# Performance work log

Hardware: AMD Instinct MI355X
Metric: run time of the kernel (lower is better)

## Reference

```python
import jax, jax.numpy as jnp
import numpy as np

N = 50000      # nodes
E = 600000     # edges
D = 128        # num_features == hidden_units
L = 4          # num_layers
C = 10         # num_classes
G = 512        # graphs in batch
BN_EPS = 1e-5


def setup_inputs() -> dict:
    key = jax.random.key(0)
    ks = jax.random.split(key, 10)
    x = jax.random.normal(ks[0], (N, D), dtype=jnp.float32)
    src = jax.random.randint(ks[1], (E,), 0, N)
    dst = jax.random.randint(ks[2], (E,), 0, N)
    edge_index = jnp.stack([src, dst]).astype(jnp.int64)
    batch = jnp.sort(jax.random.randint(ks[3], (N,), 0, G)).astype(jnp.int64)
    s = 1.0 / np.sqrt(D)
    Wc1 = jax.random.uniform(ks[4], (L, D, D), jnp.float32, -s, s)
    bc1 = jnp.zeros((L, D), jnp.float32)
    Wc2 = jax.random.uniform(ks[5], (L, D, D), jnp.float32, -s, s)
    bc2 = jnp.zeros((L, D), jnp.float32)
    g_mid = jnp.ones((L, D), jnp.float32)   # BN gamma inside conv MLP
    b_mid = jnp.zeros((L, D), jnp.float32)
    g_out = jnp.ones((L, D), jnp.float32)   # BN gamma after conv
    b_out = jnp.zeros((L, D), jnp.float32)
    fcW = jax.random.uniform(ks[6], (L + 1, D, C), jnp.float32, -s, s)
    fcb = jnp.zeros((L + 1, C), jnp.float32)
    return dict(x=x, edge_index=edge_index, batch=batch, Wc1=Wc1, bc1=bc1,
                Wc2=Wc2, bc2=bc2, g_mid=g_mid, b_mid=b_mid, g_out=g_out,
                b_out=b_out, fcW=fcW, fcb=fcb)


def _bn(h, gamma, beta):
    # training-mode BatchNorm1d over the node axis (biased variance)
    mu = h.mean(0)
    var = h.var(0)
    return (h - mu) * jax.lax.rsqrt(var + BN_EPS) * gamma + beta


def reference(x, edge_index, batch, Wc1, bc1, Wc2, bc2, g_mid, b_mid,
              g_out, b_out, fcW, fcb):
    src, dst = edge_index[0], edge_index[1]
    outs = [x]
    h = x
    for i in range(L):
        # GINConv (eps=0): nn( x + sum_{j in N(i)} x_j )
        agg = jax.ops.segment_sum(h[src], dst, num_segments=N)
        z = h + agg
        z = z @ Wc1[i] + bc1[i]
        z = jax.nn.relu(_bn(z, g_mid[i], b_mid[i]))
        z = z @ Wc2[i] + bc2[i]
        h = jax.nn.relu(_bn(z, g_out[i], b_out[i]))  # outer BN + ReLU
        outs.append(h)
    out = jnp.zeros((G, C), x.dtype)
    for i, o in enumerate(outs):
        pooled = jax.ops.segment_sum(o, batch, num_segments=G)  # [G, D]
        out = out + pooled @ fcW[i] + fcb[i]  # dropout p=0.0 -> identity
    return jax.nn.log_softmax(out, axis=-1)
```

## Files before the change

### kernel.cpp

```cpp
#include <hip/hip_runtime.h>
#include <hip/hip_bf16.h>

#define NN 50000
#define EE 600000
#define DD 128
#define LL 4
#define CC 10
#define GG 512
#define BN_EPS 1e-5f

typedef __attribute__((ext_vector_type(8))) short short8;
typedef __attribute__((ext_vector_type(4))) float f32x4;

__device__ __forceinline__ unsigned short f2b(float f) {
    union { float f; unsigned int u; } v; v.f = f;
    unsigned int u = v.u;
    unsigned int r = (u + 0x7fffu + ((u >> 16) & 1u)) >> 16;
    return (unsigned short)r;
}
__device__ __forceinline__ float b2f(unsigned short h) {
    union { unsigned int u; float f; } v; v.u = ((unsigned int)h) << 16;
    return v.f;
}


__global__ __launch_bounds__(256) void cvt_bf16(const float* __restrict__ in,
                                                unsigned short* __restrict__ out) {
    int i = blockIdx.x * 256 + threadIdx.x;
    float2 v = ((const float2*)in)[i];
    unsigned int o = (unsigned int)f2b(v.x) | ((unsigned int)f2b(v.y) << 16);
    ((unsigned int*)out)[i] = o;
}

__global__ __launch_bounds__(256) void prep_weights(const float* __restrict__ Wc1,
                                                    const float* __restrict__ Wc2,
                                                    unsigned short* __restrict__ WTb) {
    int idx = blockIdx.x * 256 + threadIdx.x;
    int mat = idx >> 14;
    int n = (idx >> 7) & 127;
    int k = idx & 127;
    const float* srcp = (mat < 4) ? (Wc1 + (size_t)mat * DD * DD)
                                  : (Wc2 + (size_t)(mat - 4) * DD * DD);
    WTb[idx] = f2b(srcp[k * DD + n]);
}


__global__ void hist_kernel(const int* __restrict__ idx, int* __restrict__ cnt, int n) {
    int i = blockIdx.x * blockDim.x + threadIdx.x;
    if (i < n) atomicAdd(&cnt[idx[i]], 1);
}

__global__ __launch_bounds__(256) void block_sums(const int* __restrict__ in,
                                                  int* __restrict__ bsums, int n) {
    __shared__ int red[256];
    int b = blockIdx.x, t = threadIdx.x;
    int base = b * 1024 + t * 4;
    int s = 0;
    if (base + 3 < n) {
        int4 v = *(const int4*)(in + base);
        s = v.x + v.y + v.z + v.w;
    } else {
        for (int i = 0; i < 4; ++i) if (base + i < n) s += in[base + i];
    }
    red[t] = s;
    __syncthreads();
    for (int off = 128; off > 0; off >>= 1) {
        if (t < off) red[t] += red[t + off];
        __syncthreads();
    }
    if (t == 0) bsums[b] = red[0];
}

__global__ __launch_bounds__(256) void scan_bsums(int* __restrict__ bsums, int nb) {
    __shared__ int red[256];
    int t = threadIdx.x;
    int v = (t < nb) ? bsums[t] : 0;
    red[t] = v;
    __syncthreads();
    for (int off = 1; off < 256; off <<= 1) {
        int u = (t >= off) ? red[t - off] : 0;
        __syncthreads();
        red[t] += u;
        __syncthreads();
    }
    if (t < nb) bsums[t] = red[t] - v;
    if (t == 0) bsums[nb] = red[255];
}

__global__ __launch_bounds__(256) void scan_final(const int* __restrict__ in,
                                                  const int* __restrict__ bsums,
                                                  int* __restrict__ out,
                                                  int* __restrict__ out2, int n) {
    __shared__ int red[256];
    int b = blockIdx.x, t = threadIdx.x;
    int base = b * 1024 + t * 4;
    int v[4];
    int s = 0;
#pragma unroll
    for (int i = 0; i < 4; ++i) {
        v[i] = (base + i < n) ? in[base + i] : 0;
        s += v[i];
    }
    red[t] = s;
    __syncthreads();
    for (int off = 1; off < 256; off <<= 1) {
        int u = (t >= off) ? red[t - off] : 0;
        __syncthreads();
        red[t] += u;
        __syncthreads();
    }
    int run = bsums[b] + red[t] - s;
#pragma unroll
    for (int i = 0; i < 4; ++i) {
        if (base + i < n) {
            out[base + i] = run;
            if (out2) out2[base + i] = run;
            run += v[i];
        }
    }
    if (b == (int)gridDim.x - 1 && t == 255) out[n] = run;
}

__global__ void fill_csr(const int* __restrict__ src, const int* __restrict__ dst,
                         int* __restrict__ cursor, int* __restrict__ csr) {
    int e = blockIdx.x * blockDim.x + threadIdx.x;
    if (e < EE) {
        int d = dst[e];
        int pos = atomicAdd(&cursor[d], 1);
        csr[pos] = src[e];
    }
}

__global__ void gptr_search(const int* __restrict__ batch, int* __restrict__ gptr) {
    int g = blockIdx.x * blockDim.x + threadIdx.x;
    if (g > GG) return;
    int lo = 0, hi = NN;
    while (lo < hi) {
        int mid = (lo + hi) >> 1;
        if (batch[mid] < g) lo = mid + 1; else hi = mid;
    }
    gptr[g] = lo;
}


template <bool BN>
__global__ __launch_bounds__(256) void aggregate_k(const unsigned short* __restrict__ hb,
                                                   const int* __restrict__ rowptr,
                                                   const int* __restrict__ csr,
                                                   const float* __restrict__ stats,
                                                   const float* __restrict__ gamma,
                                                   const float* __restrict__ beta,
                                                   unsigned short* __restrict__ outb) {
    int node = blockIdx.x * 4 + (threadIdx.x >> 6);
    if (node >= NN) return;
    int lane = threadIdx.x & 63;
    float A0 = 0.f, B0 = 0.f, A1 = 0.f, B1 = 0.f;
    if (BN) {
        int c0 = lane * 2, c1 = c0 + 1;
        float mu0 = stats[c0] * (1.0f / NN);
        float var0 = stats[DD + c0] * (1.0f / NN) - mu0 * mu0;
        A0 = gamma[c0] * rsqrtf(var0 + BN_EPS);
        B0 = beta[c0] - mu0 * A0;
        float mu1 = stats[c1] * (1.0f / NN);
        float var1 = stats[DD + c1] * (1.0f / NN) - mu1 * mu1;
        A1 = gamma[c1] * rsqrtf(var1 + BN_EPS);
        B1 = beta[c1] - mu1 * A1;
    }

    float ax, ay;
    {
        unsigned int u = ((const unsigned int*)(hb + (size_t)node * DD))[lane];
        float x = b2f((unsigned short)(u & 0xffff));
        float y = b2f((unsigned short)(u >> 16));
        if (BN) {
            x = fmaxf(0.f, fmaf(x, A0, B0));
            y = fmaxf(0.f, fmaf(y, A1, B1));
        }
        ax = x; ay = y;
    }

    int beg = rowptr[node], end = rowptr[node + 1];
    for (int e = beg; e < end; e += 8) {
        int m = end - e;
        int s[8];
#pragma unroll
        for (int i = 0; i < 8; ++i) s[i] = csr[e + ((i < m) ? i : 0)];
        unsigned int v[8];
#pragma unroll
        for (int i = 0; i < 8; ++i)
            v[i] = ((const unsigned int*)(hb + (size_t)s[i] * DD))[lane];
#pragma unroll
        for (int i = 0; i < 8; ++i) {
            if (i < m) {
                float x = b2f((unsigned short)(v[i] & 0xffff));
                float y = b2f((unsigned short)(v[i] >> 16));
                if (BN) {
                    x = fmaxf(0.f, fmaf(x, A0, B0));
                    y = fmaxf(0.f, fmaf(y, A1, B1));
                }
                ax += x; ay += y;
            }
        }
    }
    unsigned int o = (unsigned int)f2b(ax) | ((unsigned int)f2b(ay) << 16);
    ((unsigned int*)(outb + (size_t)node * DD))[lane] = o;
}


__global__ __launch_bounds__(256) void gemm_mfma(
    const unsigned short* __restrict__ Ab,
    const unsigned short* __restrict__ WTb,
    const float* __restrict__ bias,
    const float* __restrict__ bnStatsIn,
    const float* __restrict__ gamma, const float* __restrict__ beta,
    unsigned short* __restrict__ Outb,
    float* __restrict__ statsOut)
{
    __shared__ unsigned short As[128 * 128];
    __shared__ unsigned short Bs[128 * 128];
    __shared__ float AbnS[DD], BbnS[DD];
    __shared__ float colred[2][DD];

    const int tid = threadIdx.x;
    const int row0 = blockIdx.x * 128;
    const bool doBn = (bnStatsIn != nullptr);

    if (tid < DD) {
        colred[0][tid] = 0.f;
        colred[1][tid] = 0.f;
        if (doBn) {
            float mu = bnStatsIn[tid] * (1.0f / NN);
            float var = bnStatsIn[DD + tid] * (1.0f / NN) - mu * mu;
            float A = gamma[tid] * rsqrtf(var + BN_EPS);
            AbnS[tid] = A;
            BbnS[tid] = beta[tid] - mu * A;
        }
    }
    __syncthreads();

    const uint4* Bg = (const uint4*)WTb;
#pragma unroll
    for (int i = 0; i < 8; ++i) {
        int c = tid + i * 256;
        int row = c >> 4, seg = c & 15;
        uint4 v = Bg[c];
        int byte = (row * 256 + seg * 16) ^ ((row & 7) << 4);
        *(uint4*)((char*)Bs + byte) = v;
    }
#pragma unroll
    for (int i = 0; i < 8; ++i) {
        int c = tid + i * 256;
        int row = c >> 4, seg = c & 15;
        int gr = row0 + row;
        uint4 v = make_uint4(0u, 0u, 0u, 0u);
        if (gr < NN) v = ((const uint4*)(Ab + (size_t)gr * DD))[seg];
        if (doBn) {
            int k0 = seg * 8;
#pragma unroll
            for (int e = 0; e < 4; ++e) {
                unsigned int u = ((unsigned int*)&v)[e];
                int cidx = k0 + 2 * e;
                float lo = fmaxf(0.f, fmaf(b2f((unsigned short)(u & 0xffff)), AbnS[cidx], BbnS[cidx]));
                float hi = fmaxf(0.f, fmaf(b2f((unsigned short)(u >> 16)), AbnS[cidx + 1], BbnS[cidx + 1]));
                ((unsigned int*)&v)[e] = (unsigned int)f2b(lo) | ((unsigned int)f2b(hi) << 16);
            }
        }
        int byte = (row * 256 + seg * 16) ^ ((row & 7) << 4);
        *(uint4*)((char*)As + byte) = v;
    }
    __syncthreads();

    const int wave = tid >> 6, lane = tid & 63;
    const int fr = lane & 15, fq = lane >> 4;
    const int wr0 = wave * 32;

    f32x4 acc[2][8];
#pragma unroll
    for (int m = 0; m < 2; ++m)
#pragma unroll
        for (int n = 0; n < 8; ++n) acc[m][n] = (f32x4)0.f;

#pragma unroll
    for (int kk = 0; kk < 4; ++kk) {
        int kbyte = kk * 64 + fq * 16;
        short8 a[2], b[8];
#pragma unroll
        for (int m = 0; m < 2; ++m) {
            int row = wr0 + m * 16 + fr;
            a[m] = *(const short8*)((const char*)As + ((row * 256 + kbyte) ^ ((row & 7) << 4)));
        }
#pragma unroll
        for (int n = 0; n < 8; ++n) {
            int row = n * 16 + fr;
            b[n] = *(const short8*)((const char*)Bs + ((row * 256 + kbyte) ^ ((row & 7) << 4)));
        }
#pragma unroll
        for (int m = 0; m < 2; ++m)
#pragma unroll
            for (int n = 0; n < 8; ++n)
                acc[m][n] = __builtin_amdgcn_mfma_f32_16x16x32_bf16(a[m], b[n], acc[m][n], 0, 0, 0);
    }

    float bias_n[8], s[8], q[8];
#pragma unroll
    for (int n = 0; n < 8; ++n) {
        bias_n[n] = bias[n * 16 + fr];
        s[n] = 0.f;
        q[n] = 0.f;
    }
#pragma unroll
    for (int m = 0; m < 2; ++m) {
        int rbase = row0 + wr0 + m * 16 + fq * 4;
#pragma unroll
        for (int j = 0; j < 4; ++j) {
            int gr = rbase + j;
            if (gr < NN) {
#pragma unroll
                for (int n = 0; n < 8; ++n) {
                    float o = acc[m][n][j] + bias_n[n];
                    Outb[(size_t)gr * DD + n * 16 + fr] = f2b(o);
                    s[n] += o;
                    q[n] += o * o;
                }
            }
        }
    }
    if (statsOut) {
#pragma unroll
        for (int n = 0; n < 8; ++n) {
            s[n] += __shfl_xor(s[n], 16);
            s[n] += __shfl_xor(s[n], 32);
            q[n] += __shfl_xor(q[n], 16);
            q[n] += __shfl_xor(q[n], 32);
        }
        if (fq == 0) {
#pragma unroll
            for (int n = 0; n < 8; ++n) {
                atomicAdd(&colred[0][n * 16 + fr], s[n]);
                atomicAdd(&colred[1][n * 16 + fr], q[n]);
            }
        }
        __syncthreads();
        if (tid < DD) {
            atomicAdd(&statsOut[tid], colred[0][tid]);
            atomicAdd(&statsOut[DD + tid], colred[1][tid]);
        }
    }
}


__global__ __launch_bounds__(256) void bn_pool(const unsigned short* __restrict__ Z,
                                               const float* __restrict__ stats,
                                               const float* __restrict__ gamma,
                                               const float* __restrict__ beta,
                                               const int* __restrict__ gptr,
                                               float* __restrict__ pooledDst) {
    __shared__ float2 red[4][64];
    int g = blockIdx.x;
    int wave = threadIdx.x >> 6, lane = threadIdx.x & 63;
    int c0 = lane * 2, c1 = c0 + 1;
    float mu0 = stats[c0] * (1.0f / NN);
    float var0 = stats[DD + c0] * (1.0f / NN) - mu0 * mu0;
    float A0 = gamma[c0] * rsqrtf(var0 + BN_EPS);
    float B0 = beta[c0] - mu0 * A0;
    float mu1 = stats[c1] * (1.0f / NN);
    float var1 = stats[DD + c1] * (1.0f / NN) - mu1 * mu1;
    float A1 = gamma[c1] * rsqrtf(var1 + BN_EPS);
    float B1 = beta[c1] - mu1 * A1;

    float ax = 0.f, ay = 0.f;
    int beg = gptr[g], end = gptr[g + 1];
    for (int r = beg + wave; r < end; r += 4) {
        unsigned int u = ((const unsigned int*)(Z + (size_t)r * DD))[lane];
        ax += fmaxf(0.f, fmaf(b2f((unsigned short)(u & 0xffff)), A0, B0));
        ay += fmaxf(0.f, fmaf(b2f((unsigned short)(u >> 16)), A1, B1));
    }
    red[wave][lane] = make_float2(ax, ay);
    __syncthreads();
    if (threadIdx.x < 64) {
        float2 a = red[0][lane], b = red[1][lane], c = red[2][lane], d = red[3][lane];
        ((float2*)pooledDst)[(size_t)g * 64 + lane] =
            make_float2(a.x + b.x + c.x + d.x, a.y + b.y + c.y + d.y);
    }
}

__global__ __launch_bounds__(256) void pool_x(const float* __restrict__ src,
                                              const int* __restrict__ gptr,
                                              float* __restrict__ dst) {
    __shared__ float2 red[4][64];
    int g = blockIdx.x;
    int wave = threadIdx.x >> 6, lane = threadIdx.x & 63;
    float ax = 0.f, ay = 0.f;
    int beg = gptr[g], end = gptr[g + 1];
    for (int r = beg + wave; r < end; r += 4) {
        float2 v = ((const float2*)(src + (size_t)r * DD))[lane];
        ax += v.x; ay += v.y;
    }
    red[wave][lane] = make_float2(ax, ay);
    __syncthreads();
    if (threadIdx.x < 64) {
        float2 a = red[0][lane], b = red[1][lane], c = red[2][lane], d = red[3][lane];
        ((float2*)dst)[(size_t)g * 64 + lane] =
            make_float2(a.x + b.x + c.x + d.x, a.y + b.y + c.y + d.y);
    }
}


__global__ __launch_bounds__(64) void final_kernel(const float* __restrict__ pooled,
                                                   const float* __restrict__ fcW,
                                                   const float* __restrict__ fcb,
                                                   float* __restrict__ out) {
    int g = blockIdx.x;
    int lane = threadIdx.x;
    float acc[CC];
#pragma unroll
    for (int c = 0; c < CC; ++c) acc[c] = 0.f;
    for (int i = 0; i < LL + 1; ++i) {
        const float* P = pooled + ((size_t)i * GG + g) * DD;
        const float* Wf = fcW + (size_t)i * DD * CC;
        for (int k = lane; k < DD; k += 64) {
            float p = P[k];
            const float* wr = Wf + k * CC;
#pragma unroll
            for (int c = 0; c < CC; ++c) acc[c] = fmaf(p, wr[c], acc[c]);
        }
    }
#pragma unroll
    for (int c = 0; c < CC; ++c)
        for (int off = 32; off > 0; off >>= 1) acc[c] += __shfl_down(acc[c], off);
    if (lane == 0) {
#pragma unroll
        for (int c = 0; c < CC; ++c) {
            float b = 0.f;
            for (int i = 0; i < LL + 1; ++i) b += fcb[i * CC + c];
            acc[c] += b;
        }
        float m = acc[0];
#pragma unroll
        for (int c = 1; c < CC; ++c) m = fmaxf(m, acc[c]);
        float se = 0.f;
#pragma unroll
        for (int c = 0; c < CC; ++c) se += expf(acc[c] - m);
        float lse = m + logf(se);
#pragma unroll
        for (int c = 0; c < CC; ++c) out[(size_t)g * CC + c] = acc[c] - lse;
    }
}


extern "C" void kernel_launch(void* const* d_in, const int* in_sizes, int n_in,
                              void* d_out, int out_size, void* d_ws, size_t ws_size,
                              hipStream_t stream) {
    const float* x     = (const float*)d_in[0];
    const int*   ei    = (const int*)d_in[1];
    const int*   batch = (const int*)d_in[2];
    const float* Wc1   = (const float*)d_in[3];
    const float* bc1   = (const float*)d_in[4];
    const float* Wc2   = (const float*)d_in[5];
    const float* bc2   = (const float*)d_in[6];
    const float* g_mid = (const float*)d_in[7];
    const float* b_mid = (const float*)d_in[8];
    const float* g_out = (const float*)d_in[9];
    const float* b_out = (const float*)d_in[10];
    const float* fcW   = (const float*)d_in[11];
    const float* fcb   = (const float*)d_in[12];
    float* out = (float*)d_out;

    char* p = (char*)d_ws;
    unsigned short* xb   = (unsigned short*)p; p += (size_t)NN * DD * 2;
    unsigned short* aggb = (unsigned short*)p; p += (size_t)NN * DD * 2;
    unsigned short* z1b  = (unsigned short*)p; p += (size_t)NN * DD * 2;
    unsigned short* z2b  = (unsigned short*)p; p += (size_t)NN * DD * 2;
    unsigned short* WTb  = (unsigned short*)p; p += (size_t)8 * DD * DD * 2;
    float* pooled = (float*)p; p += (size_t)(LL + 1) * GG * DD * 4;
    float* statb  = (float*)p; p += 8 * 256 * 4;
    int* deg    = (int*)p; p += (size_t)NN * 4;
    int* rowptr = (int*)p; p += (size_t)(NN + 16) * 4;
    int* cursor = (int*)p; p += (size_t)NN * 4;
    int* csr    = (int*)p; p += (size_t)EE * 4;
    int* gptr   = (int*)p; p += (size_t)(GG + 16) * 4;
    int* bsum1  = (int*)p; p += 64 * 4;

    hipMemsetAsync(statb, 0, (size_t)(8 * 256) * 4 + (size_t)NN * 4, stream);

    const int* src = ei;
    const int* dst = ei + EE;

    cvt_bf16<<<(NN * DD / 2) / 256, 256, 0, stream>>>(x, xb);
    prep_weights<<<(8 * DD * DD) / 256, 256, 0, stream>>>(Wc1, Wc2, WTb);

    hist_kernel<<<(EE + 255) / 256, 256, 0, stream>>>(dst, deg, EE);
    const int nb = (NN + 1023) / 1024;
    block_sums<<<nb, 256, 0, stream>>>(deg, bsum1, NN);
    scan_bsums<<<1, 256, 0, stream>>>(bsum1, nb);
    scan_final<<<nb, 256, 0, stream>>>(deg, bsum1, rowptr, cursor, NN);
    fill_csr<<<(EE + 255) / 256, 256, 0, stream>>>(src, dst, cursor, csr);
    gptr_search<<<3, 256, 0, stream>>>(batch, gptr);
    pool_x<<<GG, 256, 0, stream>>>(x, gptr, pooled);

    const int gemmGrid = (NN + 127) / 128;
    const int aggGrid = (NN + 3) / 4;
    for (int l = 0; l < LL; ++l) {
        if (l == 0) {
            aggregate_k<false><<<aggGrid, 256, 0, stream>>>(
                xb, rowptr, csr, nullptr, nullptr, nullptr, aggb);
        } else {
            aggregate_k<true><<<aggGrid, 256, 0, stream>>>(
                z2b, rowptr, csr, statb + (size_t)(2 * (l - 1) + 1) * 256,
                g_out + (size_t)(l - 1) * DD, b_out + (size_t)(l - 1) * DD, aggb);
        }
        gemm_mfma<<<gemmGrid, 256, 0, stream>>>(
            aggb, WTb + (size_t)l * DD * DD, bc1 + (size_t)l * DD,
            nullptr, nullptr, nullptr,
            z1b, statb + (size_t)(2 * l) * 256);
        gemm_mfma<<<gemmGrid, 256, 0, stream>>>(
            z1b, WTb + (size_t)(4 + l) * DD * DD, bc2 + (size_t)l * DD,
            statb + (size_t)(2 * l) * 256, g_mid + (size_t)l * DD, b_mid + (size_t)l * DD,
            z2b, statb + (size_t)(2 * l + 1) * 256);
        bn_pool<<<GG, 256, 0, stream>>>(
            z2b, statb + (size_t)(2 * l + 1) * 256,
            g_out + (size_t)l * DD, b_out + (size_t)l * DD, gptr,
            pooled + (size_t)(l + 1) * GG * DD);
    }
    final_kernel<<<GG, 64, 0, stream>>>(pooled, fcW, fcb, out);
}
```

Baseline: 430.3 us.

## Vectorize neighbor gathers to 16B per lane and fuse x conversion into pooling

The aggregation kernel now has each wave split into four 16-lane groups. Each lane loads 16 bytes (8 bf16 channels) per neighbor, so four neighbors are in flight per wave step, and the partial sums are combined with cross-lane shuffles before one group writes the result. The aim is fewer, wider gather transactions and more memory-level parallelism per edge. The separate fp32-to-bf16 conversion of x is removed and done inside the pooling kernel, which already reads x, saving one launch and one full read of x. This assumes every node belongs to some graph range in gptr, which holds for sorted batch indices.

```diff
diff --git a/kernel.cpp b/kernel.cpp
--- a/kernel.cpp
+++ b/kernel.cpp
@@ -23,14 +23,6 @@
     return v.f;
 }
 
-
-__global__ __launch_bounds__(256) void cvt_bf16(const float* __restrict__ in,
-                                                unsigned short* __restrict__ out) {
-    int i = blockIdx.x * 256 + threadIdx.x;
-    float2 v = ((const float2*)in)[i];
-    unsigned int o = (unsigned int)f2b(v.x) | ((unsigned int)f2b(v.y) << 16);
-    ((unsigned int*)out)[i] = o;
-}
 
 __global__ __launch_bounds__(256) void prep_weights(const float* __restrict__ Wc1,
                                                     const float* __restrict__ Wc2,
@@ -153,57 +145,83 @@
                                                    unsigned short* __restrict__ outb) {
     int node = blockIdx.x * 4 + (threadIdx.x >> 6);
     if (node >= NN) return;
-    int lane = threadIdx.x & 63;
-    float A0 = 0.f, B0 = 0.f, A1 = 0.f, B1 = 0.f;
+    const int lane = threadIdx.x & 63;
+    const int seg = lane & 15;
+    const int slot = lane >> 4;
+
+    float A[8], B[8];
     if (BN) {
-        int c0 = lane * 2, c1 = c0 + 1;
-        float mu0 = stats[c0] * (1.0f / NN);
-        float var0 = stats[DD + c0] * (1.0f / NN) - mu0 * mu0;
-        A0 = gamma[c0] * rsqrtf(var0 + BN_EPS);
-        B0 = beta[c0] - mu0 * A0;
-        float mu1 = stats[c1] * (1.0f / NN);
-        float var1 = stats[DD + c1] * (1.0f / NN) - mu1 * mu1;
-        A1 = gamma[c1] * rsqrtf(var1 + BN_EPS);
-        B1 = beta[c1] - mu1 * A1;
-    }
-
-    float ax, ay;
-    {
-        unsigned int u = ((const unsigned int*)(hb + (size_t)node * DD))[lane];
-        float x = b2f((unsigned short)(u & 0xffff));
-        float y = b2f((unsigned short)(u >> 16));
-        if (BN) {
-            x = fmaxf(0.f, fmaf(x, A0, B0));
-            y = fmaxf(0.f, fmaf(y, A1, B1));
-        }
-        ax = x; ay = y;
-    }
-
-    int beg = rowptr[node], end = rowptr[node + 1];
-    for (int e = beg; e < end; e += 8) {
-        int m = end - e;
-        int s[8];
-#pragma unroll
-        for (int i = 0; i < 8; ++i) s[i] = csr[e + ((i < m) ? i : 0)];
-        unsigned int v[8];
-#pragma unroll
-        for (int i = 0; i < 8; ++i)
-            v[i] = ((const unsigned int*)(hb + (size_t)s[i] * DD))[lane];
-#pragma unroll
-        for (int i = 0; i < 8; ++i) {
-            if (i < m) {
-                float x = b2f((unsigned short)(v[i] & 0xffff));
-                float y = b2f((unsigned short)(v[i] >> 16));
-                if (BN) {
-                    x = fmaxf(0.f, fmaf(x, A0, B0));
-                    y = fmaxf(0.f, fmaf(y, A1, B1));
+#pragma unroll
+        for (int j = 0; j < 8; ++j) {
+            int c = seg * 8 + j;
+            float mu = stats[c] * (1.0f / NN);
+            float var = stats[DD + c] * (1.0f / NN) - mu * mu;
+            A[j] = gamma[c] * rsqrtf(var + BN_EPS);
+            B[j] = beta[c] - mu * A[j];
+        }
+    }
+
+    const uint4* hb4 = (const uint4*)hb;
+    uint4 self = hb4[(size_t)node * 16 + seg];
+
+    float acc[8];
+#pragma unroll
+    for (int j = 0; j < 8; ++j) acc[j] = 0.f;
+
+    const int beg = rowptr[node], end = rowptr[node + 1];
+    for (int e = beg; e < end; e += 16) {
+        int idx[4];
+        bool val[4];
+#pragma unroll
+        for (int i = 0; i < 4; ++i) {
+            int t = e + i * 4 + slot;
+            val[i] = (t < end);
+            idx[i] = csr[val[i] ? t : beg];
+        }
+        uint4 v[4];
+#pragma unroll
+        for (int i = 0; i < 4; ++i) v[i] = hb4[(size_t)idx[i] * 16 + seg];
+#pragma unroll
+        for (int i = 0; i < 4; ++i) {
+            if (val[i]) {
+#pragma unroll
+                for (int j = 0; j < 4; ++j) {
+                    unsigned int u = ((unsigned int*)&v[i])[j];
+                    float x = b2f((unsigned short)(u & 0xffff));
+                    float y = b2f((unsigned short)(u >> 16));
+                    if (BN) {
+                        x = fmaxf(0.f, fmaf(x, A[2 * j], B[2 * j]));
+                        y = fmaxf(0.f, fmaf(y, A[2 * j + 1], B[2 * j + 1]));
+                    }
+                    acc[2 * j] += x;
+                    acc[2 * j + 1] += y;
                 }
-                ax += x; ay += y;
             }
         }
     }
-    unsigned int o = (unsigned int)f2b(ax) | ((unsigned int)f2b(ay) << 16);
-    ((unsigned int*)(outb + (size_t)node * DD))[lane] = o;
+
+#pragma unroll
+    for (int j = 0; j < 8; ++j) {
+        acc[j] += __shfl_xor(acc[j], 16);
+        acc[j] += __shfl_xor(acc[j], 32);
+    }
+
+    if (slot == 0) {
+        uint4 o;
+#pragma unroll
+        for (int j = 0; j < 4; ++j) {
+            unsigned int u = ((unsigned int*)&self)[j];
+            float x = b2f((unsigned short)(u & 0xffff));
+            float y = b2f((unsigned short)(u >> 16));
+            if (BN) {
+                x = fmaxf(0.f, fmaf(x, A[2 * j], B[2 * j]));
+                y = fmaxf(0.f, fmaf(y, A[2 * j + 1], B[2 * j + 1]));
+            }
+            ((unsigned int*)&o)[j] =
+                (unsigned int)f2b(acc[2 * j] + x) | ((unsigned int)f2b(acc[2 * j + 1] + y) << 16);
+        }
+        ((uint4*)outb)[(size_t)node * 16 + seg] = o;
+    }
 }
 
 
@@ -384,17 +402,21 @@
     }
 }
 
-__global__ __launch_bounds__(256) void pool_x(const float* __restrict__ src,
-                                              const int* __restrict__ gptr,
-                                              float* __restrict__ dst) {
+
+__global__ __launch_bounds__(256) void cvt_pool_x(const float* __restrict__ x,
+                                                  const int* __restrict__ gptr,
+                                                  unsigned short* __restrict__ xb,
+                                                  float* __restrict__ dst) {
     __shared__ float2 red[4][64];
     int g = blockIdx.x;
     int wave = threadIdx.x >> 6, lane = threadIdx.x & 63;
     float ax = 0.f, ay = 0.f;
     int beg = gptr[g], end = gptr[g + 1];
     for (int r = beg + wave; r < end; r += 4) {
-        float2 v = ((const float2*)(src + (size_t)r * DD))[lane];
+        float2 v = ((const float2*)(x + (size_t)r * DD))[lane];
         ax += v.x; ay += v.y;
+        ((unsigned int*)(xb + (size_t)r * DD))[lane] =
+            (unsigned int)f2b(v.x) | ((unsigned int)f2b(v.y) << 16);
     }
     red[wave][lane] = make_float2(ax, ay);
     __syncthreads();
@@ -486,7 +508,6 @@
     const int* src = ei;
     const int* dst = ei + EE;
 
-    cvt_bf16<<<(NN * DD / 2) / 256, 256, 0, stream>>>(x, xb);
     prep_weights<<<(8 * DD * DD) / 256, 256, 0, stream>>>(Wc1, Wc2, WTb);
 
     hist_kernel<<<(EE + 255) / 256, 256, 0, stream>>>(dst, deg, EE);
@@ -496,7 +517,7 @@
     scan_final<<<nb, 256, 0, stream>>>(deg, bsum1, rowptr, cursor, NN);
     fill_csr<<<(EE + 255) / 256, 256, 0, stream>>>(src, dst, cursor, csr);
     gptr_search<<<3, 256, 0, stream>>>(batch, gptr);
-    pool_x<<<GG, 256, 0, stream>>>(x, gptr, pooled);
+    cvt_pool_x<<<GG, 256, 0, stream>>>(x, gptr, xb, pooled);
 
     const int gemmGrid = (NN + 127) / 128;
     const int aggGrid = (NN + 3) / 4;
```

Measured after the change: 418.9 us. -2.7%, faster.
